# Performance work log

Measured on AMD Instinct MI355X. Metric: run time of the kernel, lower is better.

## Reference

```python
import jax, jax.numpy as jnp
import numpy as np

N = 40000
E = 640000
IN_FEATS = 128
OUT_FEATS = 64
K = 8
FACTOR_DIM = OUT_FEATS // K  # 8
ITERATIONS = 3
TAU = 1.0
LEAKY_SLOPE = 0.01  # torch nn.LeakyReLU default


def setup_inputs() -> dict:
    key = jax.random.key(0)
    k1, k2, k3 = jax.random.split(key, 3)
    x = jax.random.normal(k1, (N, IN_FEATS), dtype=jnp.float32)
    # xavier_normal_ with gain=1.414: std = gain * sqrt(2 / (fan_in + fan_out))
    std = 1.414 * np.sqrt(2.0 / (IN_FEATS + OUT_FEATS))
    weight = jax.random.normal(k2, (IN_FEATS, OUT_FEATS), dtype=jnp.float32) * std
    bias = jnp.zeros((OUT_FEATS,), dtype=jnp.float32)
    edge_index = jax.random.randint(k3, (2, E), 0, N, dtype=jnp.int32)
    return {"x": x, "weight": weight, "bias": bias, "edge_index": edge_index}


def _l2norm(h):
    # h / ||h||_2 along last dim (no eps, matching torch code)
    return h / jnp.sqrt((h * h).sum(-1, keepdims=True))


def reference(x, weight, bias, edge_index):
    num_nodes = x.shape[0]
    src = edge_index[0]  # scatter target / softmax segment node
    dst = edge_index[1]  # gathered neighbor node

    h = jax.nn.leaky_relu(x @ weight + bias, LEAKY_SLOPE)          # [N, out]
    # split into K factors of FACTOR_DIM: [N, K, d]
    h = h.reshape(num_nodes, K, FACTOR_DIM)
    h_normed = _l2norm(h)                                           # [N, K, d]

    h_src = h_normed
    h_dst = h_normed
    for _ in range(ITERATIONS):
        feat_nbr = h_src[dst]                                       # [E, K, d]
        s = (h_dst[src] * feat_nbr).sum(-1) / TAU                   # [E, K]
        # segment softmax over edges grouped by src node
        smax = jax.ops.segment_max(s, src, num_segments=num_nodes)  # [N, K]
        ex = jnp.exp(s - smax[src])                                 # [E, K]
        denom = jax.ops.segment_sum(ex, src, num_segments=num_nodes)
        alpha = ex / denom[src]                                     # [E, K]
        msg = feat_nbr * alpha[..., None]                           # [E, K, d]
        node_attr = jax.ops.segment_sum(msg, src, num_segments=num_nodes)
        node_attr = node_attr + h_normed                            # [N, K, d]
        h_dst = _l2norm(node_attr)
    return h_dst.reshape(num_nodes, -1)                             # [N, out]
```

## Files before the change

### kernel.cpp

```cpp
#include <hip/hip_runtime.h>
#include <math.h>

#define NN   40000
#define EE   640000
#define INF_ 128
#define OUTF 64
#define SLOTS 64

#define NB8   5000
#define NCOLS 80
#define CHUNK4 2000
#define CAP   16
#define NG4  (EE / 4)

typedef float f2 __attribute__((ext_vector_type(2)));

__device__ __forceinline__ f2 pkfma(f2 a, f2 b, f2 c) {
    return __builtin_elementwise_fma(a, b, c);
}
__device__ __forceinline__ f2 shf2(f2 a, int m) {
    f2 b; b.x = __shfl_xor(a.x, m); b.y = __shfl_xor(a.y, m); return b;
}
__device__ __forceinline__ f2 bfpair(unsigned u) {
    f2 c;
    c.x = __uint_as_float(u << 16);
    c.y = __uint_as_float(u & 0xffff0000u);
    return c;
}
__device__ __forceinline__ unsigned short f2bf(float f) {
    unsigned u = __float_as_uint(f);
    return (unsigned short)((u + 0x7fffu + ((u >> 16) & 1u)) >> 16);
}
__device__ __forceinline__ float4 f4ma(float s, float4 w, float4 a) {
    a.x = fmaf(s, w.x, a.x); a.y = fmaf(s, w.y, a.y);
    a.z = fmaf(s, w.z, a.z); a.w = fmaf(s, w.w, a.w);
    return a;
}


__global__ __launch_bounds__(256) void count_gemm_k(
        const float* __restrict__ x, const float* __restrict__ w,
        const float* __restrict__ bias,
        unsigned short* __restrict__ hn16,
        const int4* __restrict__ src4, const int4* __restrict__ dst4,
        int* __restrict__ binsT, unsigned* __restrict__ csr_seg) {
    __shared__ float wl[INF_ * OUTF];

    if (blockIdx.x < NCOLS) {
        int b = blockIdx.x;
        int* lbin = (int*)wl;
        for (int i = threadIdx.x; i < NB8; i += 256) lbin[i] = 0;
        __syncthreads();
#pragma unroll
        for (int rnd = 0; rnd < 8; ++rnd) {
            int off = rnd * 256 + threadIdx.x;
            if (off < CHUNK4) {
                int gi = b * CHUNK4 + off;
                int4 s = src4[gi];
                int4 d = dst4[gi];
                int u0 = s.x >> 3, u1 = s.y >> 3, u2 = s.z >> 3, u3 = s.w >> 3;
                int r0 = atomicAdd(&lbin[u0], 1);
                int r1 = atomicAdd(&lbin[u1], 1);
                int r2 = atomicAdd(&lbin[u2], 1);
                int r3 = atomicAdd(&lbin[u3], 1);
                if (r0 < CAP) csr_seg[(u0 * NCOLS + b) * CAP + r0] = ((unsigned)d.x << 3) | (unsigned)(s.x & 7);
                if (r1 < CAP) csr_seg[(u1 * NCOLS + b) * CAP + r1] = ((unsigned)d.y << 3) | (unsigned)(s.y & 7);
                if (r2 < CAP) csr_seg[(u2 * NCOLS + b) * CAP + r2] = ((unsigned)d.z << 3) | (unsigned)(s.z & 7);
                if (r3 < CAP) csr_seg[(u3 * NCOLS + b) * CAP + r3] = ((unsigned)d.w << 3) | (unsigned)(s.w & 7);
            }
        }
        __syncthreads();
        for (int u = threadIdx.x; u < NB8; u += 256) binsT[u * NCOLS + b] = lbin[u];
        return;
    }

    for (int i = threadIdx.x; i < INF_ * OUTF; i += 256) wl[i] = w[i];
    __syncthreads();

    int wv = threadIdx.x >> 6;
    int l  = threadIdx.x & 63;
    int q  = l >> 4;
    int rr = l & 15;
    float4 bv = ((const float4*)bias)[rr];

    int nb = ((blockIdx.x - NCOLS) * 4 + wv) * 16;
    const float4* x0 = (const float4*)(x + (size_t)(nb + q     ) * INF_);
    const float4* x1 = (const float4*)(x + (size_t)(nb + q + 4 ) * INF_);
    const float4* x2 = (const float4*)(x + (size_t)(nb + q + 8 ) * INF_);
    const float4* x3 = (const float4*)(x + (size_t)(nb + q + 12) * INF_);

    float4 a0 = bv, a1 = bv, a2 = bv, a3 = bv;
#pragma unroll 2
    for (int i4 = 0; i4 < INF_ / 4; ++i4) {
        float4 v0 = x0[i4];
        float4 v1 = x1[i4];
        float4 v2 = x2[i4];
        float4 v3 = x3[i4];
        const float4* wp = ((const float4*)wl) + (i4 * 4) * 16 + rr;
        float4 w0 = wp[0], w1 = wp[16], w2 = wp[32], w3 = wp[48];
        a0 = f4ma(v0.x, w0, a0); a0 = f4ma(v0.y, w1, a0);
        a0 = f4ma(v0.z, w2, a0); a0 = f4ma(v0.w, w3, a0);
        a1 = f4ma(v1.x, w0, a1); a1 = f4ma(v1.y, w1, a1);
        a1 = f4ma(v1.z, w2, a1); a1 = f4ma(v1.w, w3, a1);
        a2 = f4ma(v2.x, w0, a2); a2 = f4ma(v2.y, w1, a2);
        a2 = f4ma(v2.z, w2, a2); a2 = f4ma(v2.w, w3, a2);
        a3 = f4ma(v3.x, w0, a3); a3 = f4ma(v3.y, w1, a3);
        a3 = f4ma(v3.z, w2, a3); a3 = f4ma(v3.w, w3, a3);
    }

    float4 acc[4] = {a0, a1, a2, a3};
#pragma unroll
    for (int k = 0; k < 4; ++k) {
        float4 a = acc[k];
        a.x = a.x > 0.f ? a.x : 0.01f * a.x;
        a.y = a.y > 0.f ? a.y : 0.01f * a.y;
        a.z = a.z > 0.f ? a.z : 0.01f * a.z;
        a.w = a.w > 0.f ? a.w : 0.01f * a.w;
        float sq = a.x*a.x + a.y*a.y + a.z*a.z + a.w*a.w;
        sq += __shfl_xor(sq, 1);
        float inv = rsqrtf(sq);
        ushort4 u;
        u.x = f2bf(a.x*inv); u.y = f2bf(a.y*inv);
        u.z = f2bf(a.z*inv); u.w = f2bf(a.w*inv);
        ((ushort4*)hn16)[(size_t)(nb + q + 4*k) * 16 + rr] = u;
    }
}


__global__ __launch_bounds__(256) void attn_build_k(const uint4* __restrict__ hg,
                                                    float* __restrict__ out,
                                                    const unsigned* __restrict__ csr_seg,
                                                    const int* __restrict__ binsT) {
    __shared__ unsigned short csr_l[8][SLOTS];
    __shared__ int cnt[8];
    __shared__ int cntc[NCOLS];

    int g = blockIdx.x;
    if (threadIdx.x < 8) cnt[threadIdx.x] = 0;
    if (threadIdx.x < NCOLS) cntc[threadIdx.x] = min(binsT[g * NCOLS + threadIdx.x], CAP);
    __syncthreads();

    const uint4* seg4 = (const uint4*)(csr_seg + (size_t)g * NCOLS * CAP);
    for (int idx4 = threadIdx.x; idx4 < NCOLS * CAP / 4; idx4 += 256) {
        int b  = idx4 >> 2;
        int s4 = idx4 & 3;
        uint4 p4 = seg4[idx4];
        int base = s4 * 4;
        int cb = cntc[b];
        if (base + 0 < cb) { int lo = (int)(p4.x & 7u); int lr = atomicAdd(&cnt[lo], 1); if (lr < SLOTS) csr_l[lo][lr] = (unsigned short)(p4.x >> 3); }
        if (base + 1 < cb) { int lo = (int)(p4.y & 7u); int lr = atomicAdd(&cnt[lo], 1); if (lr < SLOTS) csr_l[lo][lr] = (unsigned short)(p4.y >> 3); }
        if (base + 2 < cb) { int lo = (int)(p4.z & 7u); int lr = atomicAdd(&cnt[lo], 1); if (lr < SLOTS) csr_l[lo][lr] = (unsigned short)(p4.z >> 3); }
        if (base + 3 < cb) { int lo = (int)(p4.w & 7u); int lr = atomicAdd(&cnt[lo], 1); if (lr < SLOTS) csr_l[lo][lr] = (unsigned short)(p4.w >> 3); }
    }
    __syncthreads();

    int wv = threadIdx.x >> 6;
    int l  = threadIdx.x & 63;
    int pp_ = l >> 5, q = (l >> 3) & 3, r = l & 7;
    int ln = wv * 2 + pp_;
    int n  = g * 8 + ln;

    const unsigned short* row = csr_l[ln];
    int deg = min(cnt[ln], SLOTS);

    bool k0 = q      < deg;
    bool k1 = q + 4  < deg;
    bool k2 = q + 8  < deg;
    bool k3 = q + 12 < deg;
    bool k4 = q + 16 < deg;
    bool k5 = q + 20 < deg;
    bool k6 = q + 24 < deg;
    bool k7 = q + 28 < deg;
    unsigned i0 = min((unsigned)row[q     ], NN - 1u);
    unsigned i1 = min((unsigned)row[q +  4], NN - 1u);
    unsigned i2 = min((unsigned)row[q +  8], NN - 1u);
    unsigned i3 = min((unsigned)row[q + 12], NN - 1u);
    unsigned i4 = min((unsigned)row[q + 16], NN - 1u);
    unsigned i5 = min((unsigned)row[q + 20], NN - 1u);
    unsigned i6 = min((unsigned)row[q + 24], NN - 1u);
    unsigned i7 = min((unsigned)row[q + 28], NN - 1u);
    uint4 g0 = hg[(size_t)i0 * 8 + r];
    uint4 g1 = hg[(size_t)i1 * 8 + r];
    uint4 g2 = hg[(size_t)i2 * 8 + r];
    uint4 g3 = hg[(size_t)i3 * 8 + r];
    uint4 g4 = hg[(size_t)i4 * 8 + r];
    uint4 g5 = hg[(size_t)i5 * 8 + r];
    uint4 g6 = hg[(size_t)i6 * 8 + r];
    uint4 g7 = hg[(size_t)i7 * 8 + r];
    uint4 hself = hg[(size_t)n * 8 + r];

    f2 e0c0 = bfpair(g0.x), e0c1 = bfpair(g0.y), e0c2 = bfpair(g0.z), e0c3 = bfpair(g0.w);
    f2 e1c0 = bfpair(g1.x), e1c1 = bfpair(g1.y), e1c2 = bfpair(g1.z), e1c3 = bfpair(g1.w);
    f2 e2c0 = bfpair(g2.x), e2c1 = bfpair(g2.y), e2c2 = bfpair(g2.z), e2c3 = bfpair(g2.w);
    f2 e3c0 = bfpair(g3.x), e3c1 = bfpair(g3.y), e3c2 = bfpair(g3.z), e3c3 = bfpair(g3.w);
    f2 e4c0 = bfpair(g4.x), e4c1 = bfpair(g4.y), e4c2 = bfpair(g4.z), e4c3 = bfpair(g4.w);
    f2 e5c0 = bfpair(g5.x), e5c1 = bfpair(g5.y), e5c2 = bfpair(g5.z), e5c3 = bfpair(g5.w);
    f2 e6c0 = bfpair(g6.x), e6c1 = bfpair(g6.y), e6c2 = bfpair(g6.z), e6c3 = bfpair(g6.w);
    f2 e7c0 = bfpair(g7.x), e7c1 = bfpair(g7.y), e7c2 = bfpair(g7.z), e7c3 = bfpair(g7.w);

    f2 hs01 = bfpair(hself.x), hs23 = bfpair(hself.y);
    f2 hs45 = bfpair(hself.z), hs67 = bfpair(hself.w);
    f2 hd01 = hs01, hd23 = hs23, hd45 = hs45, hd67 = hs67;

    for (int it = 0; it < 3; ++it) {
        float ssum = 0.f;
        f2 A0 = {0.f, 0.f}, A1 = A0, A2 = A0, A3 = A0;

        auto proc = [&](f2 c0, f2 c1, f2 c2, f2 c3, bool ok) {
            f2 d = c0 * hd01;
            d = pkfma(c1, hd23, d);
            d = pkfma(c2, hd45, d);
            d = pkfma(c3, hd67, d);
            float dd = d.x + d.y;
            float ex = ok ? __expf(dd) : 0.f;
            ssum += ex;
            f2 exv = {ex, ex};
            A0 = pkfma(c0, exv, A0);
            A1 = pkfma(c1, exv, A1);
            A2 = pkfma(c2, exv, A2);
            A3 = pkfma(c3, exv, A3);
        };

        proc(e0c0, e0c1, e0c2, e0c3, k0);
        proc(e1c0, e1c1, e1c2, e1c3, k1);
        proc(e2c0, e2c1, e2c2, e2c3, k2);
        proc(e3c0, e3c1, e3c2, e3c3, k3);
        proc(e4c0, e4c1, e4c2, e4c3, k4);
        proc(e5c0, e5c1, e5c2, e5c3, k5);
        proc(e6c0, e6c1, e6c2, e6c3, k6);
        proc(e7c0, e7c1, e7c2, e7c3, k7);

        for (int e = 32 + q; e < deg; e += 4) {
            unsigned ii = min((unsigned)row[e], NN - 1u);
            uint4 gg = hg[(size_t)ii * 8 + r];
            proc(bfpair(gg.x), bfpair(gg.y), bfpair(gg.z), bfpair(gg.w), true);
        }

#pragma unroll
        for (int m = 8; m < 32; m <<= 1) {
            ssum += __shfl_xor(ssum, m);
            A0 += shf2(A0, m);
            A1 += shf2(A1, m);
            A2 += shf2(A2, m);
            A3 += shf2(A3, m);
        }

        float rs = (ssum > 0.f) ? 1.f / ssum : 0.f;
        f2 rsv = {rs, rs};
        f2 t01 = pkfma(A0, rsv, hs01);
        f2 t23 = pkfma(A1, rsv, hs23);
        f2 t45 = pkfma(A2, rsv, hs45);
        f2 t67 = pkfma(A3, rsv, hs67);
        f2 d = t01 * t01;
        d = pkfma(t23, t23, d);
        d = pkfma(t45, t45, d);
        d = pkfma(t67, t67, d);
        float inv = rsqrtf(d.x + d.y);
        f2 iv = {inv, inv};
        hd01 = t01 * iv; hd23 = t23 * iv; hd45 = t45 * iv; hd67 = t67 * iv;
    }

    if (q == 0) {
        float4* o4 = (float4*)(out + (size_t)n * OUTF + r * 8);
        o4[0] = make_float4(hd01.x, hd01.y, hd23.x, hd23.y);
        o4[1] = make_float4(hd45.x, hd45.y, hd67.x, hd67.y);
    }
}


extern "C" void kernel_launch(void* const* d_in, const int* in_sizes, int n_in,
                              void* d_out, int out_size, void* d_ws, size_t ws_size,
                              hipStream_t stream) {
    const float* x    = (const float*)d_in[0];
    const float* w    = (const float*)d_in[1];
    const float* bias = (const float*)d_in[2];
    const int*   ei   = (const int*)d_in[3];
    const int*   src  = ei;
    const int*   dst  = ei + EE;
    float* out = (float*)d_out;

    char* ws = (char*)d_ws;
    size_t off = 0;
    unsigned short* hn16    = (unsigned short*)(ws + off); off += (size_t)NN * OUTF * 2;
    int*            binsT   = (int*)(ws + off);            off += (size_t)NB8 * NCOLS * 4;
    unsigned*       csr_seg = (unsigned*)(ws + off);       off += (size_t)NB8 * NCOLS * CAP * 4;
    (void)ws_size; (void)in_sizes; (void)n_in; (void)out_size;

    count_gemm_k<<<NCOLS + 625, 256, 0, stream>>>(
        x, w, bias, hn16, (const int4*)src, (const int4*)dst, binsT, csr_seg);

    attn_build_k<<<NB8, 256, 0, stream>>>((const uint4*)hn16, out,
                                          csr_seg, binsT);
}
```

Baseline: 61.80 us.

## Replace fixed-capacity edge bins with compact per-column counting-sort partitions

```diff
diff --git a/kernel.cpp b/kernel.cpp
--- a/kernel.cpp
+++ b/kernel.cpp
@@ -10,7 +10,7 @@
 #define NB8   5000
 #define NCOLS 80
 #define CHUNK4 2000
-#define CAP   16
+#define COLE  8000
 #define NG4  (EE / 4)
 
 typedef float f2 __attribute__((ext_vector_type(2)));
@@ -43,34 +43,73 @@
         const float* __restrict__ bias,
         unsigned short* __restrict__ hn16,
         const int4* __restrict__ src4, const int4* __restrict__ dst4,
-        int* __restrict__ binsT, unsigned* __restrict__ csr_seg) {
+        int* __restrict__ binsT, int* __restrict__ binsO,
+        unsigned* __restrict__ part) {
     __shared__ float wl[INF_ * OUTF];
 
     if (blockIdx.x < NCOLS) {
         int b = blockIdx.x;
-        int* lbin = (int*)wl;
-        for (int i = threadIdx.x; i < NB8; i += 256) lbin[i] = 0;
+        int* cnt  = (int*)wl;
+        int* tsum = (int*)wl + 5120;
+        for (int i = threadIdx.x; i < NB8; i += 256) cnt[i] = 0;
         __syncthreads();
 #pragma unroll
         for (int rnd = 0; rnd < 8; ++rnd) {
             int off = rnd * 256 + threadIdx.x;
             if (off < CHUNK4) {
-                int gi = b * CHUNK4 + off;
-                int4 s = src4[gi];
-                int4 d = dst4[gi];
-                int u0 = s.x >> 3, u1 = s.y >> 3, u2 = s.z >> 3, u3 = s.w >> 3;
-                int r0 = atomicAdd(&lbin[u0], 1);
-                int r1 = atomicAdd(&lbin[u1], 1);
-                int r2 = atomicAdd(&lbin[u2], 1);
-                int r3 = atomicAdd(&lbin[u3], 1);
-                if (r0 < CAP) csr_seg[(u0 * NCOLS + b) * CAP + r0] = ((unsigned)d.x << 3) | (unsigned)(s.x & 7);
-                if (r1 < CAP) csr_seg[(u1 * NCOLS + b) * CAP + r1] = ((unsigned)d.y << 3) | (unsigned)(s.y & 7);
-                if (r2 < CAP) csr_seg[(u2 * NCOLS + b) * CAP + r2] = ((unsigned)d.z << 3) | (unsigned)(s.z & 7);
-                if (r3 < CAP) csr_seg[(u3 * NCOLS + b) * CAP + r3] = ((unsigned)d.w << 3) | (unsigned)(s.w & 7);
+                int4 s = src4[b * CHUNK4 + off];
+                atomicAdd(&cnt[s.x >> 3], 1);
+                atomicAdd(&cnt[s.y >> 3], 1);
+                atomicAdd(&cnt[s.z >> 3], 1);
+                atomicAdd(&cnt[s.w >> 3], 1);
             }
         }
         __syncthreads();
-        for (int u = threadIdx.x; u < NB8; u += 256) binsT[u * NCOLS + b] = lbin[u];
+        for (int g = threadIdx.x; g < NB8; g += 256) binsT[b * NB8 + g] = cnt[g];
+        __syncthreads();
+        int base = threadIdx.x * 20;
+        int s = 0;
+        if (base < NB8) {
+#pragma unroll
+            for (int k = 0; k < 20; ++k) s += cnt[base + k];
+        }
+        tsum[threadIdx.x] = s;
+        __syncthreads();
+        for (int off = 1; off < 256; off <<= 1) {
+            int t = (threadIdx.x >= off) ? tsum[threadIdx.x - off] : 0;
+            __syncthreads();
+            tsum[threadIdx.x] += t;
+            __syncthreads();
+        }
+        int run = tsum[threadIdx.x] - s;
+        if (base < NB8) {
+#pragma unroll
+            for (int k = 0; k < 20; ++k) {
+                int c = cnt[base + k];
+                cnt[base + k] = run;
+                run += c;
+            }
+        }
+        __syncthreads();
+        for (int g = threadIdx.x; g < NB8; g += 256) binsO[b * NB8 + g] = cnt[g];
+        __syncthreads();
+        unsigned* pw = part + (size_t)b * COLE;
+#pragma unroll
+        for (int rnd = 0; rnd < 8; ++rnd) {
+            int off = rnd * 256 + threadIdx.x;
+            if (off < CHUNK4) {
+                int4 sE = src4[b * CHUNK4 + off];
+                int4 dE = dst4[b * CHUNK4 + off];
+                int p0 = atomicAdd(&cnt[sE.x >> 3], 1);
+                int p1 = atomicAdd(&cnt[sE.y >> 3], 1);
+                int p2 = atomicAdd(&cnt[sE.z >> 3], 1);
+                int p3 = atomicAdd(&cnt[sE.w >> 3], 1);
+                pw[p0] = ((unsigned)dE.x << 3) | (unsigned)(sE.x & 7);
+                pw[p1] = ((unsigned)dE.y << 3) | (unsigned)(sE.y & 7);
+                pw[p2] = ((unsigned)dE.z << 3) | (unsigned)(sE.z & 7);
+                pw[p3] = ((unsigned)dE.w << 3) | (unsigned)(sE.w & 7);
+            }
+        }
         return;
     }
 
@@ -129,28 +168,27 @@
 
 __global__ __launch_bounds__(256) void attn_build_k(const uint4* __restrict__ hg,
                                                     float* __restrict__ out,
-                                                    const unsigned* __restrict__ csr_seg,
-                                                    const int* __restrict__ binsT) {
+                                                    const unsigned* __restrict__ part,
+                                                    const int* __restrict__ binsT,
+                                                    const int* __restrict__ binsO) {
     __shared__ unsigned short csr_l[8][SLOTS];
-    __shared__ int cnt[8];
-    __shared__ int cntc[NCOLS];
+    __shared__ int cnt8[8];
 
     int g = blockIdx.x;
-    if (threadIdx.x < 8) cnt[threadIdx.x] = 0;
-    if (threadIdx.x < NCOLS) cntc[threadIdx.x] = min(binsT[g * NCOLS + threadIdx.x], CAP);
+    if (threadIdx.x < 8) cnt8[threadIdx.x] = 0;
     __syncthreads();
 
-    const uint4* seg4 = (const uint4*)(csr_seg + (size_t)g * NCOLS * CAP);
-    for (int idx4 = threadIdx.x; idx4 < NCOLS * CAP / 4; idx4 += 256) {
-        int b  = idx4 >> 2;
-        int s4 = idx4 & 3;
-        uint4 p4 = seg4[idx4];
-        int base = s4 * 4;
-        int cb = cntc[b];
-        if (base + 0 < cb) { int lo = (int)(p4.x & 7u); int lr = atomicAdd(&cnt[lo], 1); if (lr < SLOTS) csr_l[lo][lr] = (unsigned short)(p4.x >> 3); }
-        if (base + 1 < cb) { int lo = (int)(p4.y & 7u); int lr = atomicAdd(&cnt[lo], 1); if (lr < SLOTS) csr_l[lo][lr] = (unsigned short)(p4.y >> 3); }
-        if (base + 2 < cb) { int lo = (int)(p4.z & 7u); int lr = atomicAdd(&cnt[lo], 1); if (lr < SLOTS) csr_l[lo][lr] = (unsigned short)(p4.z >> 3); }
-        if (base + 3 < cb) { int lo = (int)(p4.w & 7u); int lr = atomicAdd(&cnt[lo], 1); if (lr < SLOTS) csr_l[lo][lr] = (unsigned short)(p4.w >> 3); }
+    if (threadIdx.x < NCOLS) {
+        int b = threadIdx.x;
+        int c = binsT[b * NB8 + g];
+        int o = binsO[b * NB8 + g];
+        const unsigned* pp = part + (size_t)b * COLE + o;
+        for (int k = 0; k < c; ++k) {
+            unsigned p = pp[k];
+            int lo = (int)(p & 7u);
+            int lr = atomicAdd(&cnt8[lo], 1);
+            if (lr < SLOTS) csr_l[lo][lr] = (unsigned short)(p >> 3);
+        }
     }
     __syncthreads();
 
@@ -161,7 +199,7 @@
     int n  = g * 8 + ln;
 
     const unsigned short* row = csr_l[ln];
-    int deg = min(cnt[ln], SLOTS);
+    int deg = min(cnt8[ln], SLOTS);
 
     bool k0 = q      < deg;
     bool k1 = q + 4  < deg;
@@ -281,14 +319,15 @@
 
     char* ws = (char*)d_ws;
     size_t off = 0;
-    unsigned short* hn16    = (unsigned short*)(ws + off); off += (size_t)NN * OUTF * 2;
-    int*            binsT   = (int*)(ws + off);            off += (size_t)NB8 * NCOLS * 4;
-    unsigned*       csr_seg = (unsigned*)(ws + off);       off += (size_t)NB8 * NCOLS * CAP * 4;
+    unsigned short* hn16  = (unsigned short*)(ws + off); off += (size_t)NN * OUTF * 2;
+    int*            binsT = (int*)(ws + off);            off += (size_t)NCOLS * NB8 * 4;
+    int*            binsO = (int*)(ws + off);            off += (size_t)NCOLS * NB8 * 4;
+    unsigned*       part  = (unsigned*)(ws + off);       off += (size_t)EE * 4;
     (void)ws_size; (void)in_sizes; (void)n_in; (void)out_size;
 
     count_gemm_k<<<NCOLS + 625, 256, 0, stream>>>(
-        x, w, bias, hn16, (const int4*)src, (const int4*)dst, binsT, csr_seg);
+        x, w, bias, hn16, (const int4*)src, (const int4*)dst, binsT, binsO, part);
 
     attn_build_k<<<NB8, 256, 0, stream>>>((const uint4*)hn16, out,
-                                          csr_seg, binsT);
-}
+                                          part, binsT, binsO);
+}
```

New measurement: 63.53 us. 1.03x slower.
